# Optimization experiments

Measured on AMD Instinct MI355X. Metric: run time of the kernel, lower is better.

## Reference

```python
import jax, jax.numpy as jnp
import numpy as np

EPS = 0.0001


def setup_inputs() -> dict:
    key = jax.random.key(0)
    k1, k2, k3, k4, k5 = jax.random.split(key, 5)
    N, H, V = 65536, 48, 96
    return {
        "point": jax.random.normal(k1, (N, 3), dtype=jnp.float32),
        "hyperplane_A": jax.random.normal(k2, (N, H, 3), dtype=jnp.float32),
        "hyperplane_b": jax.random.normal(k3, (N, H, 1), dtype=jnp.float32),
        "v1": jax.random.normal(k4, (N, V, 3), dtype=jnp.float32),
        "v2": jax.random.normal(k5, (N, V, 3), dtype=jnp.float32),
    }


def reference(point, hyperplane_A, hyperplane_b, v1, v2):
    # point: [N,3]; hyperplane_A: [N,H,3]; hyperplane_b: [N,H,1]; v1,v2: [N,V,3]
    A = hyperplane_A
    b = hyperplane_b[..., 0]                                   # [N,H]
    inf = jnp.inf

    # --- signed facet offsets ---
    Apb = jnp.einsum("nhd,nd->nh", A, point) - b               # [N,H]
    Apb = jnp.where(jnp.isfinite(Apb), Apb, -inf)              # inf/nan -> -inf

    is_neg = jnp.all(Apb <= 0, axis=-1)                        # [N] point inside zonotope
    neg_dist = jnp.max(Apb, axis=-1)                           # [N]
    neg_idx = jnp.argmax(Apb, axis=-1)                         # [N]
    neg_grad = jnp.take_along_axis(A, neg_idx[:, None, None], axis=1)[:, 0]  # [N,3]

    # --- face (perpendicular) distances, computed densely for all points ---
    proj = point[:, None, :] - Apb[..., None] * A              # [N,H,3] projections onto planes
    App = jnp.einsum("nkd,nhd->nhk", A, proj) - b[:, None, :]  # [N,H,K] all planes vs each projection
    App = jnp.where(jnp.isfinite(App), App, -inf)
    on_zono = jnp.all(App <= EPS, axis=-1)                     # [N,H] projection lies on the zonotope
    perp = jnp.linalg.norm(point[:, None, :] - proj, axis=-1)  # [N,H]
    perp = jnp.where(on_zono, perp, inf)
    perp = jnp.where(jnp.isnan(perp), inf, perp)
    face_dist = jnp.min(perp, axis=-1)                         # [N]
    face_idx = jnp.argmin(perp, axis=-1)
    face_grad = jnp.take_along_axis(A, face_idx[:, None, None], axis=1)[:, 0]  # [N,3]

    # --- edge (segment) distances ---
    d = v2 - v1                                                # [N,V,3]
    denom = jnp.sum(d * d, axis=-1, keepdims=True)             # [N,V,1]
    t_hat = jnp.sum((point[:, None, :] - v1) * d, axis=-1, keepdims=True) / denom
    t_star = jnp.clip(t_hat, 0.0, 1.0)
    v = v1 + t_star * d                                        # [N,V,3] closest point on segment
    ed = jnp.linalg.norm(point[:, None, :] - v, axis=-1)       # [N,V]
    ed = jnp.where(jnp.isnan(ed), inf, ed)
    edge_dist = jnp.min(ed, axis=-1)                           # [N]
    edge_idx = jnp.argmin(ed, axis=-1)
    v_min = jnp.take_along_axis(v, edge_idx[:, None, None], axis=1)[:, 0]  # [N,3]
    edge_grad = (point - v_min) / edge_dist[:, None]           # [N,3]

    # --- combine: edge beats face; inside-points use max facet offset ---
    use_edge = edge_dist < face_dist                           # [N]
    nn_dist = jnp.where(use_edge, edge_dist, face_dist)
    nn_grad = jnp.where(use_edge[:, None], edge_grad, face_grad)

    distances = jnp.where(is_neg, neg_dist, nn_dist)           # [N]
    gradients = jnp.where(is_neg[:, None], neg_grad, nn_grad)  # [N,3]
    return distances[:, None], gradients
```

## Files before the change

### kernel.cpp

```cpp
#include <hip/hip_runtime.h>
#include <math.h>
#include <float.h>


typedef float f32x2 __attribute__((ext_vector_type(2)));
typedef float f4u   __attribute__((ext_vector_type(4), aligned(4)));
typedef unsigned long long u64;
typedef unsigned int u32;

constexpr int H = 48;
constexpr int V = 96;
constexpr int WPB = 4;
constexpr int PPW = 4;
constexpr float ZEPS = 1e-4f;

__device__ __forceinline__ f32x2 pkmul(f32x2 a, f32x2 b) {
  f32x2 d;
  asm("v_pk_mul_f32 %0, %1, %2" : "=v"(d) : "v"(a), "v"(b));
  return d;
}
__device__ __forceinline__ f32x2 pkadd(f32x2 a, f32x2 b) {
  f32x2 d;
  asm("v_pk_add_f32 %0, %1, %2" : "=v"(d) : "v"(a), "v"(b));
  return d;
}
__device__ __forceinline__ f32x2 pksub(f32x2 a, f32x2 b) {
  f32x2 d;
  asm("v_pk_add_f32 %0, %1, %2 neg_lo:[0,1] neg_hi:[0,1]" : "=v"(d) : "v"(a), "v"(b));
  return d;
}
__device__ __forceinline__ float max3f(float a, float b, float c) {
  float d;
  asm("v_max3_f32 %0, %1, %2, %3" : "=v"(d) : "v"(a), "v"(b), "v"(c));
  return d;
}

__global__ __launch_bounds__(256, 4) void zono_dist_kernel(
    const float* __restrict__ point,
    const float* __restrict__ Ag,
    const float* __restrict__ bg,
    const float* __restrict__ v1g,
    const float* __restrict__ v2g,
    float* __restrict__ out,
    int N)
{
#pragma clang fp contract(off)
  __shared__ __align__(16) float sQ[WPB][3][PPW][56];

  const int wave = threadIdx.x >> 6;
  const int lane = threadIdx.x & 63;
  const int g = lane >> 4;
  const int j = lane & 15;
  int n = blockIdx.x * (WPB * PPW) + wave * PPW + g;
  if (n >= N) n = N - 1;

  const float px = point[3 * (size_t)n + 0];
  const float py = point[3 * (size_t)n + 1];
  const float pz = point[3 * (size_t)n + 2];

  const float* ap = Ag + (size_t)n * (H * 3) + 9 * j;
  f4u A0 = *(const f4u*)(ap);
  f4u A1 = *(const f4u*)(ap + 4);
  const float a2z = ap[8];
  const float* bp = bg + (size_t)n * H + 3 * j;
  const float b0 = bp[0], b1 = bp[1], b2 = bp[2];

  const float* e1p = v1g + (size_t)n * (V * 3) + 18 * j;
  const float* e2p = v2g + (size_t)n * (V * 3) + 18 * j;
  f4u Ea = *(const f4u*)(e1p);      f4u Eb = *(const f4u*)(e1p + 4);
  f4u Ec = *(const f4u*)(e1p + 8);  f4u Ed = *(const f4u*)(e1p + 12);
  f32x2 Ee = *(const f32x2*)(e1p + 16);
  f4u Fa = *(const f4u*)(e2p);      f4u Fb = *(const f4u*)(e2p + 4);
  f4u Fc = *(const f4u*)(e2p + 8);  f4u Fd = *(const f4u*)(e2p + 12);
  f32x2 Fe = *(const f32x2*)(e2p + 16);

  const float ax0 = A0.x, ay0 = A0.y, az0 = A0.z;
  const float ax1 = A0.w, ay1 = A1.x, az1 = A1.y;
  const float ax2 = A1.z, ay2 = A1.w, az2 = a2z;

  const float apb0 = ((ax0 * px + ay0 * py) + az0 * pz) - b0;
  const float apb1 = ((ax1 * px + ay1 * py) + az1 * pz) - b1;
  const float apb2 = ((ax2 * px + ay2 * py) + az2 * pz) - b2;
  const float q0x = px - apb0 * ax0, q0y = py - apb0 * ay0, q0z = pz - apb0 * az0;
  const float q1x = px - apb1 * ax1, q1y = py - apb1 * ay1, q1z = pz - apb1 * az1;
  const float q2x = px - apb2 * ax2, q2y = py - apb2 * ay2, q2z = pz - apb2 * az2;

  float* qxw = &sQ[wave][0][g][0];
  float* qyw = &sQ[wave][1][g][0];
  float* qzw = &sQ[wave][2][g][0];
  qxw[3 * j + 0] = q0x; qxw[3 * j + 1] = q1x; qxw[3 * j + 2] = q2x;
  qyw[3 * j + 0] = q0y; qyw[3 * j + 1] = q1y; qyw[3 * j + 2] = q2y;
  qzw[3 * j + 0] = q0z; qzw[3 * j + 1] = q1z; qzw[3 * j + 2] = q2z;

  const u64 bneg = __ballot(max3f(apb0, apb1, apb2) <= 0.0f);
  u32 negbits = 0;
  if ((bneg & 0x000000000000FFFFull) == 0x000000000000FFFFull) negbits |= 1;
  if ((bneg & 0x00000000FFFF0000ull) == 0x00000000FFFF0000ull) negbits |= 2;
  if ((bneg & 0x0000FFFF00000000ull) == 0x0000FFFF00000000ull) negbits |= 4;
  if ((bneg & 0xFFFF000000000000ull) == 0xFFFF000000000000ull) negbits |= 8;

  const f32x2 AX0 = {ax0, ax0}, AY0 = {ay0, ay0}, AZ0 = {az0, az0}, B0 = {b0, b0};
  const f32x2 AX1 = {ax1, ax1}, AY1 = {ay1, ay1}, AZ1 = {az1, az1}, B1 = {b1, b1};
  const f32x2 AX2 = {ax2, ax2}, AY2 = {ay2, ay2}, AZ2 = {az2, az2}, B2 = {b2, b2};

  u64 bad0 = 0, bad1 = 0, bad2 = 0, bad3 = 0;
  const f32x2* qxp = (const f32x2*)qxw;
  const f32x2* qyp = (const f32x2*)qyw;
  const f32x2* qzp = (const f32x2*)qzw;
  #pragma unroll
  for (int hp = 0; hp < 24; ++hp) {
    const f32x2 QX = qxp[hp], QY = qyp[hp], QZ = qzp[hp];
    f32x2 s0 = pksub(pkadd(pkadd(pkmul(AX0, QX), pkmul(AY0, QY)), pkmul(AZ0, QZ)), B0);
    f32x2 s1 = pksub(pkadd(pkadd(pkmul(AX1, QX), pkmul(AY1, QY)), pkmul(AZ1, QZ)), B1);
    f32x2 s2 = pksub(pkadd(pkadd(pkmul(AX2, QX), pkmul(AY2, QY)), pkmul(AZ2, QZ)), B2);
    const u64 bl0 = __ballot(max3f(s0.x, s1.x, s2.x) <= ZEPS);
    const u64 bl1 = __ballot(max3f(s0.y, s1.y, s2.y) <= ZEPS);
    const u64 c0 = 1ull << (2 * hp), c1 = 1ull << (2 * hp + 1);
    bad0 |= ((~bl0 & 0x000000000000FFFFull) ? c0 : 0) | ((~bl1 & 0x000000000000FFFFull) ? c1 : 0);
    bad1 |= ((~bl0 & 0x00000000FFFF0000ull) ? c0 : 0) | ((~bl1 & 0x00000000FFFF0000ull) ? c1 : 0);
    bad2 |= ((~bl0 & 0x0000FFFF00000000ull) ? c0 : 0) | ((~bl1 & 0x0000FFFF00000000ull) ? c1 : 0);
    bad3 |= ((~bl0 & 0xFFFF000000000000ull) ? c0 : 0) | ((~bl1 & 0xFFFF000000000000ull) ? c1 : 0);
  }
  const u64 MASK48 = (1ull << H) - 1;
  const bool anyface = (((~bad0) | (~bad1) | (~bad2) | (~bad3)) & MASK48) != 0;

  float fv = INFINITY, fgx = 0.f, fgy = 0.f, fgz = 0.f;
  if (anyface) {
    const u64 badg = (g == 0) ? bad0 : (g == 1) ? bad1 : (g == 2) ? bad2 : bad3;
    const u32 mb = (u32)(badg >> (3 * j));
    float p0 = INFINITY, p1 = INFINITY, p2 = INFINITY;
    if (!(mb & 1)) {
      float dx = px - q0x, dy = py - q0y, dz = pz - q0z;
      p0 = sqrtf((dx * dx + dy * dy) + dz * dz);
    }
    if (!(mb & 2)) {
      float dx = px - q1x, dy = py - q1y, dz = pz - q1z;
      p1 = sqrtf((dx * dx + dy * dy) + dz * dz);
    }
    if (!(mb & 4)) {
      float dx = px - q2x, dy = py - q2y, dz = pz - q2z;
      p2 = sqrtf((dx * dx + dy * dy) + dz * dz);
    }
    float bv = p0; int bk = 0;
    if (p1 < bv) { bv = p1; bk = 1; }
    if (p2 < bv) { bv = p2; bk = 2; }
    u64 key = ((u64)__float_as_uint(bv) << 16) | (u32)(3 * j + bk);
    #pragma unroll
    for (int off = 8; off; off >>= 1) {
      u64 o = __shfl_xor(key, off);
      if (o < key) key = o;
    }
    fv = __uint_as_float((u32)(key >> 16));
    const int ks = (int)(key & 0xFFFF);
    const int owner = 16 * g + ks / 3;
    const int ms = ks - 3 * (ks / 3);
    const float sx0 = __shfl(ax0, owner), sx1 = __shfl(ax1, owner), sx2 = __shfl(ax2, owner);
    const float sy0 = __shfl(ay0, owner), sy1 = __shfl(ay1, owner), sy2 = __shfl(ay2, owner);
    const float sz0 = __shfl(az0, owner), sz1 = __shfl(az1, owner), sz2 = __shfl(az2, owner);
    fgx = (ms == 0) ? sx0 : (ms == 1) ? sx1 : sx2;
    fgy = (ms == 0) ? sy0 : (ms == 1) ? sy1 : sy2;
    fgz = (ms == 0) ? sz0 : (ms == 1) ? sz1 : sz2;
  }

  float nv = 0.f, ngx = 0.f, ngy = 0.f, ngz = 0.f;
  if (negbits) {
    float bv = apb0; int bk = 0;
    if (apb1 > bv) { bv = apb1; bk = 1; }
    if (apb2 > bv) { bv = apb2; bk = 2; }
    u32 bits = __float_as_uint(bv);
    u32 obits = (bits >> 31) ? ~bits : (bits | 0x80000000u);
    u64 key = ((u64)obits << 16) | (u32)(0xFFFF - (3 * j + bk));
    #pragma unroll
    for (int off = 8; off; off >>= 1) {
      u64 o = __shfl_xor(key, off);
      if (o > key) key = o;
    }
    const int ks = (int)(0xFFFF - (key & 0xFFFF));
    const int owner = 16 * g + ks / 3;
    const int ms = ks - 3 * (ks / 3);
    const float v0 = __shfl(apb0, owner), v1 = __shfl(apb1, owner), v2 = __shfl(apb2, owner);
    nv = (ms == 0) ? v0 : (ms == 1) ? v1 : v2;
    const float sx0 = __shfl(ax0, owner), sx1 = __shfl(ax1, owner), sx2 = __shfl(ax2, owner);
    const float sy0 = __shfl(ay0, owner), sy1 = __shfl(ay1, owner), sy2 = __shfl(ay2, owner);
    const float sz0 = __shfl(az0, owner), sz1 = __shfl(az1, owner), sz2 = __shfl(az2, owner);
    ngx = (ms == 0) ? sx0 : (ms == 1) ? sx1 : sx2;
    ngy = (ms == 0) ? sy0 : (ms == 1) ? sy1 : sy2;
    ngz = (ms == 0) ? sz0 : (ms == 1) ? sz1 : sz2;
  }

  const float u[18] = {Ea.x, Ea.y, Ea.z, Ea.w, Eb.x, Eb.y, Eb.z, Eb.w,
                       Ec.x, Ec.y, Ec.z, Ec.w, Ed.x, Ed.y, Ed.z, Ed.w,
                       Ee.x, Ee.y};
  const float w[18] = {Fa.x, Fa.y, Fa.z, Fa.w, Fb.x, Fb.y, Fb.z, Fb.w,
                       Fc.x, Fc.y, Fc.z, Fc.w, Fd.x, Fd.y, Fd.z, Fd.w,
                       Fe.x, Fe.y};
  float bed = INFINITY, bvx = 0.f, bvy = 0.f, bvz = 0.f;
  int bte = 0;
  #pragma unroll
  for (int t = 0; t < 6; ++t) {
    const float x1 = u[3 * t], y1 = u[3 * t + 1], z1 = u[3 * t + 2];
    const float x2 = w[3 * t], y2 = w[3 * t + 1], z2 = w[3 * t + 2];
    const float dx = x2 - x1, dy = y2 - y1, dz = z2 - z1;
    const float den = (dx * dx + dy * dy) + dz * dz;
    const float wx = px - x1, wy = py - y1, wz = pz - z1;
    const float th = ((wx * dx + wy * dy) + wz * dz) / den;
    const float ts = th < 0.0f ? 0.0f : (th > 1.0f ? 1.0f : th);
    const float vx = x1 + ts * dx, vy = y1 + ts * dy, vz = z1 + ts * dz;
    const float ex = px - vx, ey = py - vy, ez = pz - vz;
    const float ed = sqrtf((ex * ex + ey * ey) + ez * ez);
    if (ed < bed) { bed = ed; bte = t; bvx = vx; bvy = vy; bvz = vz; }
  }
  u64 ekey = ((u64)__float_as_uint(bed) << 16) | (u32)(6 * j + bte);
  #pragma unroll
  for (int off = 8; off; off >>= 1) {
    u64 o = __shfl_xor(ekey, off);
    if (o < ekey) ekey = o;
  }
  const float m = __uint_as_float((u32)(ekey >> 16));
  const int el = (int)(ekey & 0xFFFF);
  const int wl = 16 * g + el / 6;
  const float wvx = __shfl(bvx, wl);
  const float wvy = __shfl(bvy, wl);
  const float wvz = __shfl(bvz, wl);

  const bool isneg = (negbits >> g) & 1;
  const bool use_edge = (m < fv);
  const float pd = (j == 0) ? px : (j == 1) ? py : pz;
  const float wd = (j == 0) ? wvx : (j == 1) ? wvy : wvz;
  const float fd = (j == 0) ? fgx : (j == 1) ? fgy : fgz;
  const float nd = (j == 0) ? ngx : (j == 1) ? ngy : ngz;
  float dist, gnum, gden = 1.0f;
  if (isneg) {
    dist = nv; gnum = nd;
  } else if (use_edge) {
    dist = m; gnum = pd - wd; gden = m;
  } else {
    dist = fv; gnum = fd;
  }
  const float gr = gnum / gden;
  if (j < 3) out[(size_t)N + 3 * (size_t)n + j] = gr;
  if (j == 3) out[n] = dist;
}

extern "C" void kernel_launch(void* const* d_in, const int* in_sizes, int n_in,
                              void* d_out, int out_size, void* d_ws, size_t ws_size,
                              hipStream_t stream) {
  const float* point = (const float*)d_in[0];
  const float* Ag    = (const float*)d_in[1];
  const float* bg    = (const float*)d_in[2];
  const float* v1g   = (const float*)d_in[3];
  const float* v2g   = (const float*)d_in[4];
  float* out = (float*)d_out;

  const int N = in_sizes[0] / 3;
  const int ppb = WPB * PPW;
  const int blocks = (N + ppb - 1) / ppb;
  zono_dist_kernel<<<blocks, WPB * 64, 0, stream>>>(point, Ag, bg, v1g, v2g, out, N);
}
```

Baseline: 46.53 us.

## Process two points per lane group to overlap loads with compute

Each wave now handles two sets of points. All loads for the first point are issued together with the hyperplane loads for the second, and the edge loads for the second point are issued before the first point's compute, so memory latency can overlap with arithmetic. The grid shrinks by half. The projections are now reread from shared memory instead of held in registers. The cost is higher register pressure under the 4-waves-per-SIMD launch bound, which may cause spills, and fewer blocks to hide latency. A dead, unused compute_point stub is also left in the file.

```diff
diff --git a/kernel.cpp b/kernel.cpp
--- a/kernel.cpp
+++ b/kernel.cpp
@@ -35,63 +35,50 @@
   return d;
 }
 
-__global__ __launch_bounds__(256, 4) void zono_dist_kernel(
-    const float* __restrict__ point,
-    const float* __restrict__ Ag,
-    const float* __restrict__ bg,
-    const float* __restrict__ v1g,
-    const float* __restrict__ v2g,
-    float* __restrict__ out,
-    int N)
+struct Edges { f4u a, b, c, d; f32x2 e; };
+__device__ __forceinline__ Edges load18(const float* p) {
+  Edges r;
+  r.a = *(const f4u*)(p);
+  r.b = *(const f4u*)(p + 4);
+  r.c = *(const f4u*)(p + 8);
+  r.d = *(const f4u*)(p + 12);
+  r.e = *(const f32x2*)(p + 16);
+  return r;
+}
+
+__device__ __forceinline__ void phase_q(
+    int j, float px, float py, float pz,
+    float ax0, float ay0, float az0, float ax1, float ay1, float az1,
+    float ax2, float ay2, float az2, float b0, float b1, float b2,
+    float* qxw, float* qyw, float* qzw,
+    float& apb0, float& apb1, float& apb2)
 {
 #pragma clang fp contract(off)
-  __shared__ __align__(16) float sQ[WPB][3][PPW][56];
-
-  const int wave = threadIdx.x >> 6;
-  const int lane = threadIdx.x & 63;
-  const int g = lane >> 4;
-  const int j = lane & 15;
-  int n = blockIdx.x * (WPB * PPW) + wave * PPW + g;
-  if (n >= N) n = N - 1;
-
-  const float px = point[3 * (size_t)n + 0];
-  const float py = point[3 * (size_t)n + 1];
-  const float pz = point[3 * (size_t)n + 2];
-
-  const float* ap = Ag + (size_t)n * (H * 3) + 9 * j;
-  f4u A0 = *(const f4u*)(ap);
-  f4u A1 = *(const f4u*)(ap + 4);
-  const float a2z = ap[8];
-  const float* bp = bg + (size_t)n * H + 3 * j;
-  const float b0 = bp[0], b1 = bp[1], b2 = bp[2];
-
-  const float* e1p = v1g + (size_t)n * (V * 3) + 18 * j;
-  const float* e2p = v2g + (size_t)n * (V * 3) + 18 * j;
-  f4u Ea = *(const f4u*)(e1p);      f4u Eb = *(const f4u*)(e1p + 4);
-  f4u Ec = *(const f4u*)(e1p + 8);  f4u Ed = *(const f4u*)(e1p + 12);
-  f32x2 Ee = *(const f32x2*)(e1p + 16);
-  f4u Fa = *(const f4u*)(e2p);      f4u Fb = *(const f4u*)(e2p + 4);
-  f4u Fc = *(const f4u*)(e2p + 8);  f4u Fd = *(const f4u*)(e2p + 12);
-  f32x2 Fe = *(const f32x2*)(e2p + 16);
-
-  const float ax0 = A0.x, ay0 = A0.y, az0 = A0.z;
-  const float ax1 = A0.w, ay1 = A1.x, az1 = A1.y;
-  const float ax2 = A1.z, ay2 = A1.w, az2 = a2z;
-
-  const float apb0 = ((ax0 * px + ay0 * py) + az0 * pz) - b0;
-  const float apb1 = ((ax1 * px + ay1 * py) + az1 * pz) - b1;
-  const float apb2 = ((ax2 * px + ay2 * py) + az2 * pz) - b2;
-  const float q0x = px - apb0 * ax0, q0y = py - apb0 * ay0, q0z = pz - apb0 * az0;
-  const float q1x = px - apb1 * ax1, q1y = py - apb1 * ay1, q1z = pz - apb1 * az1;
-  const float q2x = px - apb2 * ax2, q2y = py - apb2 * ay2, q2z = pz - apb2 * az2;
-
-  float* qxw = &sQ[wave][0][g][0];
-  float* qyw = &sQ[wave][1][g][0];
-  float* qzw = &sQ[wave][2][g][0];
-  qxw[3 * j + 0] = q0x; qxw[3 * j + 1] = q1x; qxw[3 * j + 2] = q2x;
-  qyw[3 * j + 0] = q0y; qyw[3 * j + 1] = q1y; qyw[3 * j + 2] = q2y;
-  qzw[3 * j + 0] = q0z; qzw[3 * j + 1] = q1z; qzw[3 * j + 2] = q2z;
-
+  apb0 = ((ax0 * px + ay0 * py) + az0 * pz) - b0;
+  apb1 = ((ax1 * px + ay1 * py) + az1 * pz) - b1;
+  apb2 = ((ax2 * px + ay2 * py) + az2 * pz) - b2;
+  qxw[3 * j + 0] = px - apb0 * ax0;
+  qxw[3 * j + 1] = px - apb1 * ax1;
+  qxw[3 * j + 2] = px - apb2 * ax2;
+  qyw[3 * j + 0] = py - apb0 * ay0;
+  qyw[3 * j + 1] = py - apb1 * ay1;
+  qyw[3 * j + 2] = py - apb2 * ay2;
+  qzw[3 * j + 0] = pz - apb0 * az0;
+  qzw[3 * j + 1] = pz - apb1 * az1;
+  qzw[3 * j + 2] = pz - apb2 * az2;
+}
+
+__device__ __forceinline__ void compute_point(
+    int n, int g, int j, int N,
+    float px, float py, float pz,
+    float ax0, float ay0, float az0, float ax1, float ay1, float az1,
+    float ax2, float ay2, float az2,
+    float apb0, float apb1, float apb2,
+    const Edges& E, const Edges& F,
+    const float* qxw, const float* qyw, const float* qzw,
+    float* __restrict__ out)
+{
+#pragma clang fp contract(off)
   const u64 bneg = __ballot(max3f(apb0, apb1, apb2) <= 0.0f);
   u32 negbits = 0;
   if ((bneg & 0x000000000000FFFFull) == 0x000000000000FFFFull) negbits |= 1;
@@ -99,10 +86,38 @@
   if ((bneg & 0x0000FFFF00000000ull) == 0x0000FFFF00000000ull) negbits |= 4;
   if ((bneg & 0xFFFF000000000000ull) == 0xFFFF000000000000ull) negbits |= 8;
 
-  const f32x2 AX0 = {ax0, ax0}, AY0 = {ay0, ay0}, AZ0 = {az0, az0}, B0 = {b0, b0};
-  const f32x2 AX1 = {ax1, ax1}, AY1 = {ay1, ay1}, AZ1 = {az1, az1}, B1 = {b1, b1};
-  const f32x2 AX2 = {ax2, ax2}, AY2 = {ay2, ay2}, AZ2 = {az2, az2}, B2 = {b2, b2};
-
+  const f32x2 AX0 = {ax0, ax0}, AY0 = {ay0, ay0}, AZ0 = {az0, az0}, B0 = {0, 0};
+  const f32x2 AX1 = {ax1, ax1}, AY1 = {ay1, ay1}, AZ1 = {az1, az1};
+  const f32x2 AX2 = {ax2, ax2}, AY2 = {ay2, ay2}, AZ2 = {az2, az2};
+  (void)B0;
+  u64 bad0 = 0, bad1 = 0, bad2 = 0, bad3 = 0;
+  {
+  }
+  (void)bad0; (void)bad1; (void)bad2; (void)bad3;
+}
+
+__device__ __forceinline__ void compute_point_full(
+    int n, int g, int j, int N,
+    float px, float py, float pz,
+    float ax0, float ay0, float az0, float ax1, float ay1, float az1,
+    float ax2, float ay2, float az2,
+    float b0, float b1, float b2,
+    float apb0, float apb1, float apb2,
+    const Edges& E, const Edges& F,
+    const float* qxw, const float* qyw, const float* qzw,
+    float* __restrict__ out)
+{
+#pragma clang fp contract(off)
+  const u64 bneg = __ballot(max3f(apb0, apb1, apb2) <= 0.0f);
+  u32 negbits = 0;
+  if ((bneg & 0x000000000000FFFFull) == 0x000000000000FFFFull) negbits |= 1;
+  if ((bneg & 0x00000000FFFF0000ull) == 0x00000000FFFF0000ull) negbits |= 2;
+  if ((bneg & 0x0000FFFF00000000ull) == 0x0000FFFF00000000ull) negbits |= 4;
+  if ((bneg & 0xFFFF000000000000ull) == 0xFFFF000000000000ull) negbits |= 8;
+
+  const f32x2 AX0 = {ax0, ax0}, AY0 = {ay0, ay0}, AZ0 = {az0, az0}, PB0 = {b0, b0};
+  const f32x2 AX1 = {ax1, ax1}, AY1 = {ay1, ay1}, AZ1 = {az1, az1}, PB1 = {b1, b1};
+  const f32x2 AX2 = {ax2, ax2}, AY2 = {ay2, ay2}, AZ2 = {az2, az2}, PB2 = {b2, b2};
   u64 bad0 = 0, bad1 = 0, bad2 = 0, bad3 = 0;
   const f32x2* qxp = (const f32x2*)qxw;
   const f32x2* qyp = (const f32x2*)qyw;
@@ -110,9 +125,9 @@
   #pragma unroll
   for (int hp = 0; hp < 24; ++hp) {
     const f32x2 QX = qxp[hp], QY = qyp[hp], QZ = qzp[hp];
-    f32x2 s0 = pksub(pkadd(pkadd(pkmul(AX0, QX), pkmul(AY0, QY)), pkmul(AZ0, QZ)), B0);
-    f32x2 s1 = pksub(pkadd(pkadd(pkmul(AX1, QX), pkmul(AY1, QY)), pkmul(AZ1, QZ)), B1);
-    f32x2 s2 = pksub(pkadd(pkadd(pkmul(AX2, QX), pkmul(AY2, QY)), pkmul(AZ2, QZ)), B2);
+    f32x2 s0 = pksub(pkadd(pkadd(pkmul(AX0, QX), pkmul(AY0, QY)), pkmul(AZ0, QZ)), PB0);
+    f32x2 s1 = pksub(pkadd(pkadd(pkmul(AX1, QX), pkmul(AY1, QY)), pkmul(AZ1, QZ)), PB1);
+    f32x2 s2 = pksub(pkadd(pkadd(pkmul(AX2, QX), pkmul(AY2, QY)), pkmul(AZ2, QZ)), PB2);
     const u64 bl0 = __ballot(max3f(s0.x, s1.x, s2.x) <= ZEPS);
     const u64 bl1 = __ballot(max3f(s0.y, s1.y, s2.y) <= ZEPS);
     const u64 c0 = 1ull << (2 * hp), c1 = 1ull << (2 * hp + 1);
@@ -128,6 +143,9 @@
   if (anyface) {
     const u64 badg = (g == 0) ? bad0 : (g == 1) ? bad1 : (g == 2) ? bad2 : bad3;
     const u32 mb = (u32)(badg >> (3 * j));
+    const float q0x = qxw[3 * j + 0], q1x = qxw[3 * j + 1], q2x = qxw[3 * j + 2];
+    const float q0y = qyw[3 * j + 0], q1y = qyw[3 * j + 1], q2y = qyw[3 * j + 2];
+    const float q0z = qzw[3 * j + 0], q1z = qzw[3 * j + 1], q2z = qzw[3 * j + 2];
     float p0 = INFINITY, p1 = INFINITY, p2 = INFINITY;
     if (!(mb & 1)) {
       float dx = px - q0x, dy = py - q0y, dz = pz - q0z;
@@ -188,12 +206,12 @@
     ngz = (ms == 0) ? sz0 : (ms == 1) ? sz1 : sz2;
   }
 
-  const float u[18] = {Ea.x, Ea.y, Ea.z, Ea.w, Eb.x, Eb.y, Eb.z, Eb.w,
-                       Ec.x, Ec.y, Ec.z, Ec.w, Ed.x, Ed.y, Ed.z, Ed.w,
-                       Ee.x, Ee.y};
-  const float w[18] = {Fa.x, Fa.y, Fa.z, Fa.w, Fb.x, Fb.y, Fb.z, Fb.w,
-                       Fc.x, Fc.y, Fc.z, Fc.w, Fd.x, Fd.y, Fd.z, Fd.w,
-                       Fe.x, Fe.y};
+  const float u[18] = {E.a.x, E.a.y, E.a.z, E.a.w, E.b.x, E.b.y, E.b.z, E.b.w,
+                       E.c.x, E.c.y, E.c.z, E.c.w, E.d.x, E.d.y, E.d.z, E.d.w,
+                       E.e.x, E.e.y};
+  const float w[18] = {F.a.x, F.a.y, F.a.z, F.a.w, F.b.x, F.b.y, F.b.z, F.b.w,
+                       F.c.x, F.c.y, F.c.z, F.c.w, F.d.x, F.d.y, F.d.z, F.d.w,
+                       F.e.x, F.e.y};
   float bed = INFINITY, bvx = 0.f, bvy = 0.f, bvz = 0.f;
   int bte = 0;
   #pragma unroll
@@ -242,6 +260,84 @@
   if (j == 3) out[n] = dist;
 }
 
+__global__ __launch_bounds__(256, 4) void zono_dist_kernel(
+    const float* __restrict__ point,
+    const float* __restrict__ Ag,
+    const float* __restrict__ bg,
+    const float* __restrict__ v1g,
+    const float* __restrict__ v2g,
+    float* __restrict__ out,
+    int N)
+{
+#pragma clang fp contract(off)
+  __shared__ __align__(16) float sQ[WPB][2][3][PPW][56];
+
+  const int wave = threadIdx.x >> 6;
+  const int lane = threadIdx.x & 63;
+  const int g = lane >> 4;
+  const int j = lane & 15;
+  int n0 = blockIdx.x * (WPB * PPW * 2) + wave * (PPW * 2) + g;
+  int n1 = n0 + PPW;
+  if (n0 >= N) n0 = N - 1;
+  if (n1 >= N) n1 = N - 1;
+
+  const float p0x = point[3 * (size_t)n0 + 0];
+  const float p0y = point[3 * (size_t)n0 + 1];
+  const float p0z = point[3 * (size_t)n0 + 2];
+  const float* ap0 = Ag + (size_t)n0 * (H * 3) + 9 * j;
+  f4u A00 = *(const f4u*)(ap0);
+  f4u A01 = *(const f4u*)(ap0 + 4);
+  const float a0z2 = ap0[8];
+  const float* bp0 = bg + (size_t)n0 * H + 3 * j;
+  const float b00 = bp0[0], b01 = bp0[1], b02 = bp0[2];
+  const Edges E0 = load18(v1g + (size_t)n0 * (V * 3) + 18 * j);
+  const Edges F0 = load18(v2g + (size_t)n0 * (V * 3) + 18 * j);
+
+  const float p1x = point[3 * (size_t)n1 + 0];
+  const float p1y = point[3 * (size_t)n1 + 1];
+  const float p1z = point[3 * (size_t)n1 + 2];
+  const float* ap1 = Ag + (size_t)n1 * (H * 3) + 9 * j;
+  f4u A10 = *(const f4u*)(ap1);
+  f4u A11 = *(const f4u*)(ap1 + 4);
+  const float a1z2 = ap1[8];
+  const float* bp1 = bg + (size_t)n1 * H + 3 * j;
+  const float b10 = bp1[0], b11 = bp1[1], b12 = bp1[2];
+
+  const float ax00 = A00.x, ay00 = A00.y, az00 = A00.z;
+  const float ax01 = A00.w, ay01 = A01.x, az01 = A01.y;
+  const float ax02 = A01.z, ay02 = A01.w, az02 = a0z2;
+  const float ax10 = A10.x, ay10 = A10.y, az10 = A10.z;
+  const float ax11 = A10.w, ay11 = A11.x, az11 = A11.y;
+  const float ax12 = A11.z, ay12 = A11.w, az12 = a1z2;
+
+  float* q0xw = &sQ[wave][0][0][g][0];
+  float* q0yw = &sQ[wave][0][1][g][0];
+  float* q0zw = &sQ[wave][0][2][g][0];
+  float* q1xw = &sQ[wave][1][0][g][0];
+  float* q1yw = &sQ[wave][1][1][g][0];
+  float* q1zw = &sQ[wave][1][2][g][0];
+
+  float apb00, apb01, apb02, apb10, apb11, apb12;
+  phase_q(j, p0x, p0y, p0z, ax00, ay00, az00, ax01, ay01, az01,
+          ax02, ay02, az02, b00, b01, b02, q0xw, q0yw, q0zw,
+          apb00, apb01, apb02);
+  phase_q(j, p1x, p1y, p1z, ax10, ay10, az10, ax11, ay11, az11,
+          ax12, ay12, az12, b10, b11, b12, q1xw, q1yw, q1zw,
+          apb10, apb11, apb12);
+
+  const Edges E1 = load18(v1g + (size_t)n1 * (V * 3) + 18 * j);
+  const Edges F1 = load18(v2g + (size_t)n1 * (V * 3) + 18 * j);
+
+  compute_point_full(n0, g, j, N, p0x, p0y, p0z,
+                     ax00, ay00, az00, ax01, ay01, az01, ax02, ay02, az02,
+                     b00, b01, b02, apb00, apb01, apb02,
+                     E0, F0, q0xw, q0yw, q0zw, out);
+  compute_point_full(n1, g, j, N, p1x, p1y, p1z,
+                     ax10, ay10, az10, ax11, ay11, az11, ax12, ay12, az12,
+                     b10, b11, b12, apb10, apb11, apb12,
+                     E1, F1, q1xw, q1yw, q1zw, out);
+}
+
 extern "C" void kernel_launch(void* const* d_in, const int* in_sizes, int n_in,
                               void* d_out, int out_size, void* d_ws, size_t ws_size,
                               hipStream_t stream) {
@@ -253,7 +349,7 @@
   float* out = (float*)d_out;
 
   const int N = in_sizes[0] / 3;
-  const int ppb = WPB * PPW;
+  const int ppb = WPB * PPW * 2;
   const int blocks = (N + ppb - 1) / ppb;
   zono_dist_kernel<<<blocks, WPB * 64, 0, stream>>>(point, Ag, bg, v1g, v2g, out, N);
 }
```

Result: slower. 67.25 us (+44.5%).
